# Kernel tuning notes

Hardware: AMD Instinct MI355X
Metric: run time of the kernel (lower is better)

Reference implementation:

```python
import jax, jax.numpy as jnp
import numpy as np

B, S, L, DM, DP, H, HT, NO = 1, 64, 256, 256, 128, 8, 4, 32
EPS = 1e-5


def _lin(key, din, dout):
    k1, k2 = jax.random.split(key)
    s = 1.0 / np.sqrt(din)
    w = jax.random.uniform(k1, (din, dout), minval=-s, maxval=s, dtype=jnp.float32)
    b = jax.random.uniform(k2, (dout,), minval=-s, maxval=s, dtype=jnp.float32)
    return w, b


def setup_inputs() -> dict:
    key = jax.random.key(0)
    ks = jax.random.split(key, 16)
    inp = {}
    inp['msa'] = jax.random.normal(ks[0], (B, S, L, DM), dtype=jnp.float32)
    inp['pair'] = jax.random.normal(ks[1], (B, L, L, DP), dtype=jnp.float32)
    # row attention
    inp['row_norm_g'] = jnp.ones((DM,), jnp.float32); inp['row_norm_b'] = jnp.zeros((DM,), jnp.float32)
    inp['row_qkv_w'], inp['row_qkv_b'] = _lin(ks[2], DM, 3 * DM)
    inp['row_out_w'], inp['row_out_b'] = _lin(ks[3], DM, DM)
    # column attention
    inp['col_norm_g'] = jnp.ones((DM,), jnp.float32); inp['col_norm_b'] = jnp.zeros((DM,), jnp.float32)
    inp['col_qkv_w'], inp['col_qkv_b'] = _lin(ks[4], DM, 3 * DM)
    inp['col_out_w'], inp['col_out_b'] = _lin(ks[5], DM, DM)
    inp['ff_norm_g'] = jnp.ones((DM,), jnp.float32); inp['ff_norm_b'] = jnp.zeros((DM,), jnp.float32)
    inp['ff_w1'], inp['ff_b1'] = _lin(ks[6], DM, 4 * DM)
    inp['ff_w2'], inp['ff_b2'] = _lin(ks[7], 4 * DM, DM)
    # outer product mean
    inp['op_norm_g'] = jnp.ones((DM,), jnp.float32); inp['op_norm_b'] = jnp.zeros((DM,), jnp.float32)
    inp['op_a_w'], inp['op_a_b'] = _lin(ks[8], DM, NO)
    inp['op_b_w'], inp['op_b_b'] = _lin(ks[9], DM, NO)
    inp['op_out_w'], inp['op_out_b'] = _lin(ks[10], NO * NO, DP)
    # triangle attention
    inp['tri_norm_g'] = jnp.ones((DP,), jnp.float32); inp['tri_norm_b'] = jnp.zeros((DP,), jnp.float32)
    inp['tri_qkv_w'], inp['tri_qkv_b'] = _lin(ks[11], DP, 3 * DP)
    inp['tri_out_w'], inp['tri_out_b'] = _lin(ks[12], DP, DP)
    return inp


def layer_norm(x, g, b):
    m = jnp.mean(x, axis=-1, keepdims=True)
    v = jnp.mean(jnp.square(x - m), axis=-1, keepdims=True)
    return (x - m) * jax.lax.rsqrt(v + EPS) * g + b


def mha(x, qkv_w, qkv_b, out_w, out_b, n_heads):
    # x: (..., n, d); attention over axis n. Dropout is eval-mode (identity).
    *lead, n, d = x.shape
    hd = d // n_heads
    qkv = x @ qkv_w + qkv_b
    q, k, v = jnp.split(qkv, 3, axis=-1)
    q = q.reshape(*lead, n, n_heads, hd)
    k = k.reshape(*lead, n, n_heads, hd)
    v = v.reshape(*lead, n, n_heads, hd)
    attn = jnp.einsum('...ihd,...jhd->...hij', q, k) * (hd ** -0.5)
    attn = jnp.clip(attn, -50.0, 50.0)
    attn = jax.nn.softmax(attn, axis=-1)
    out = jnp.einsum('...hij,...jhd->...ihd', attn, v).reshape(*lead, n, d)
    return out @ out_w + out_b


def reference(msa, pair,
              row_norm_g, row_norm_b, row_qkv_w, row_qkv_b, row_out_w, row_out_b,
              col_norm_g, col_norm_b, col_qkv_w, col_qkv_b, col_out_w, col_out_b,
              ff_norm_g, ff_norm_b, ff_w1, ff_b1, ff_w2, ff_b2,
              op_norm_g, op_norm_b, op_a_w, op_a_b, op_b_w, op_b_b, op_out_w, op_out_b,
              tri_norm_g, tri_norm_b, tri_qkv_w, tri_qkv_b, tri_out_w, tri_out_b):
    # row attention over seq_len axis
    msa = msa + mha(layer_norm(msa, row_norm_g, row_norm_b),
                    row_qkv_w, row_qkv_b, row_out_w, row_out_b, H)
    # column attention: transpose (b s n d) -> (b n s d), attend over n_seqs
    msa_t = jnp.swapaxes(msa, 1, 2)
    msa_t = msa_t + mha(layer_norm(msa_t, col_norm_g, col_norm_b),
                        col_qkv_w, col_qkv_b, col_out_w, col_out_b, H)
    msa = jnp.swapaxes(msa_t, 1, 2)
    # feed-forward
    h = layer_norm(msa, ff_norm_g, ff_norm_b)
    msa = msa + (jax.nn.relu(h @ ff_w1 + ff_b1) @ ff_w2 + ff_b2)
    # outer product mean: msa -> pair update
    m = layer_norm(msa, op_norm_g, op_norm_b)
    a = m @ op_a_w + op_a_b   # (b, s, L, NO)
    b_ = m @ op_b_w + op_b_b  # (b, s, L, NO)
    n_seqs = msa.shape[1]
    outer = jnp.einsum('bsic,bsjd->bijcd', a, b_) / float(n_seqs)  # (b, L, L, NO, NO)
    bsz, Ld = outer.shape[0], outer.shape[1]
    pair = pair + outer.reshape(bsz, Ld, Ld, NO * NO) @ op_out_w + op_out_b
    # triangle attention (row-wise attention over last L axis, 4 heads)
    pn = layer_norm(pair, tri_norm_g, tri_norm_b)
    pair = pair + mha(pn, tri_qkv_w, tri_qkv_b, tri_out_w, tri_out_b, HT)
    return msa, pair
```

## Files before the change

kernel.cpp:

```cpp
#include <hip/hip_runtime.h>
#include <hip/hip_bf16.h>


#define S_ 64
#define L_ 256
#define DM_ 256
#define DP_ 128
#define H_ 8
#define HT_ 4
#define NO_ 32

typedef __hip_bfloat16 bf16;
typedef short short4s __attribute__((ext_vector_type(4)));
typedef short short8 __attribute__((ext_vector_type(8)));
typedef float floatx4 __attribute__((ext_vector_type(4)));

__device__ __forceinline__ short f2bfs(float x) {
  union { float f; unsigned u; } v;
  v.f = x;
  unsigned r = (v.u + 0x7fffu + ((v.u >> 16) & 1u)) >> 16;
  return (short)r;
}

__global__ void k_ln(const float* __restrict__ src, bf16* __restrict__ dst,
                     const float* __restrict__ g, const float* __restrict__ bta, int D) {
  int row = blockIdx.x * 4 + (threadIdx.x >> 6);
  const float* x = src + (size_t)row * D;
  bf16* y = dst + (size_t)row * D;
  int t = threadIdx.x & 63;
  float v[4];
  int cnt = 0;
  float sum = 0.f;
  for (int e = t; e < D; e += 64) { float xv = x[e]; v[cnt++] = xv; sum += xv; }
  #pragma unroll
  for (int o = 32; o; o >>= 1) sum += __shfl_down(sum, o);
  sum = __shfl(sum, 0);
  float mean = sum / D;
  float var = 0.f;
  for (int k = 0; k < cnt; k++) { float d = v[k] - mean; var += d * d; }
  #pragma unroll
  for (int o = 32; o; o >>= 1) var += __shfl_down(var, o);
  var = __shfl(var, 0);
  float rstd = rsqrtf(var / D + 1e-5f);
  cnt = 0;
  for (int e = t; e < D; e += 64)
    y[e] = __float2bfloat16((v[cnt++] - mean) * rstd * g[e] + bta[e]);
}

struct WtJob { const float* W; bf16* Wt; int K; int N; int nblk; };
struct WtJobs { WtJob j[10]; };

__global__ void k_wt_all(WtJobs jobs) {
  __shared__ float tile[32][33];
  int b = blockIdx.x;
  int ji = 0;
  while (ji < 9 && b >= jobs.j[ji].nblk) { b -= jobs.j[ji].nblk; ji++; }
  const float* W = jobs.j[ji].W;
  bf16* Wt = jobs.j[ji].Wt;
  int K = jobs.j[ji].K, N = jobs.j[ji].N;
  int kt = K >> 5;
  int k0 = (b % kt) * 32, n0 = (b / kt) * 32;
  int tid = threadIdx.x;
  for (int e = tid; e < 1024; e += 256) {
    int r = e >> 5, c = e & 31;
    tile[r][c] = W[(size_t)(k0 + r) * N + (n0 + c)];
  }
  __syncthreads();
  for (int e = tid; e < 1024; e += 256) {
    int r = e >> 5, c = e & 31;
    Wt[(size_t)(n0 + r) * K + (k0 + c)] = __float2bfloat16(tile[c][r]);
  }
}

__global__ void k_wtopm(const float* __restrict__ W, bf16* __restrict__ Wt,
                        const float* __restrict__ ba, const float* __restrict__ bb,
                        float* __restrict__ bias_ab) {
  if (blockIdx.x == 0 && threadIdx.x < 64)
    bias_ab[threadIdx.x] = threadIdx.x < 32 ? ba[threadIdx.x] : bb[threadIdx.x - 32];
  int idx = blockIdx.x * 256 + threadIdx.x;
  int d = idx >> 10, kk = idx & 1023;
  int e = kk >> 5, c = kk & 31;
  Wt[idx] = __float2bfloat16(W[(size_t)(c * 32 + e) * 128 + d]);
}

__global__ void k_topm(const bf16* __restrict__ ab, bf16* __restrict__ a_t,
                       bf16* __restrict__ b_t) {
  __shared__ bf16 tile[64][34];
  int i = blockIdx.x;
  int y = blockIdx.y;
  bf16* out = y ? b_t : a_t;
  int tid = threadIdx.x;
  for (int e = tid; e < 64 * 32; e += 256) {
    int s = e >> 5, c = e & 31;
    tile[s][c] = ab[((size_t)s * L_ + i) * 64 + y * 32 + c];
  }
  __syncthreads();
  for (int e = tid; e < 64 * 32; e += 256) {
    int c = e >> 6, s = e & 63;
    out[((size_t)i * NO_ + c) * S_ + s] = tile[s][c];
  }
}

template<int MODE, int LNF>
__global__ void k_gemm64(const bf16* __restrict__ A, const bf16* __restrict__ Wt,
                         const float* __restrict__ bias, float* __restrict__ Cf,
                         bf16* __restrict__ Cb, const float* __restrict__ Csrc,
                         float* __restrict__ Cdup, int M, int N, int K, float scale,
                         const float* __restrict__ Af = nullptr,
                         const float* __restrict__ lng = nullptr,
                         const float* __restrict__ lnbt = nullptr) {
  __shared__ short As[64 * 64];
  __shared__ short Bs[64 * 64];
  __shared__ float sMean[64];
  __shared__ float sRstd[64];
  const int tid = threadIdx.x;
  const int nwg = gridDim.x * gridDim.y;
  const int wgid = blockIdx.y * gridDim.x + blockIdx.x;
  const int q = nwg >> 3, r8 = nwg & 7;
  const int xcd = wgid & 7, loc = wgid >> 3;
  const int swz = (xcd < r8 ? xcd * (q + 1) : r8 * (q + 1) + (xcd - r8) * q) + loc;
  const int by = swz / gridDim.x, bx = swz - by * gridDim.x;
  const int m0 = by * 64, n0 = bx * 64;
  const int w = tid >> 6, l = tid & 63;
  const int wm = (w >> 1) * 32, wn = (w & 1) * 32;
  const int lr = l & 15, lk = l >> 4;

  if (LNF) {
    int rr = tid >> 2, quad = tid & 3;
    const float* xr = Af + (size_t)(m0 + rr) * 256 + quad * 64;
    float s = 0.f, s2 = 0.f;
    #pragma unroll
    for (int ii = 0; ii < 16; ii++) {
      floatx4 x = *(const floatx4*)(xr + ii * 4);
      #pragma unroll
      for (int jj = 0; jj < 4; jj++) { s += x[jj]; s2 += x[jj] * x[jj]; }
    }
    #pragma unroll
    for (int o = 1; o <= 2; o <<= 1) { s += __shfl_xor(s, o); s2 += __shfl_xor(s2, o); }
    if (quad == 0) {
      float mean = s * 0.00390625f;
      float var = s2 * 0.00390625f - mean * mean;
      sMean[rr] = mean;
      sRstd[rr] = rsqrtf(var + 1e-5f);
    }
    __syncthreads();
  }

  floatx4 acc[2][2] = {};
  const short* Ash = (const short*)A;
  const short* Bsh = (const short*)Wt;
  for (int k0 = 0; k0 < K; k0 += 64) {
    if (LNF) {
      for (int e = tid; e < 512; e += 256) {
        int r = e >> 3, kg = e & 7;
        int kb = k0 + kg * 8;
        const float* src = Af + (size_t)(m0 + r) * 256 + kb;
        floatx4 x0 = *(const floatx4*)(src);
        floatx4 x1 = *(const floatx4*)(src + 4);
        float mean = sMean[r], rstd = sRstd[r];
        short8 v;
        #pragma unroll
        for (int jj = 0; jj < 4; jj++) {
          v[jj] = f2bfs((x0[jj] - mean) * rstd * lng[kb + jj] + lnbt[kb + jj]);
          v[jj + 4] = f2bfs((x1[jj] - mean) * rstd * lng[kb + 4 + jj] + lnbt[kb + 4 + jj]);
        }
        *(short8*)(&As[r * 64 + ((kg ^ (r & 7)) * 8)]) = v;
      }
    } else {
      for (int e = tid; e < 512; e += 256) {
        int r = e >> 3, kg = e & 7;
        short8 v = *(const short8*)(Ash + (size_t)(m0 + r) * K + k0 + kg * 8);
        *(short8*)(&As[r * 64 + ((kg ^ (r & 7)) * 8)]) = v;
      }
    }
    for (int e = tid; e < 512; e += 256) {
      int r = e >> 3, kg = e & 7;
      int n = n0 + r;
      short8 v = {0, 0, 0, 0, 0, 0, 0, 0};
      if (n < N) v = *(const short8*)(Bsh + (size_t)n * K + k0 + kg * 8);
      *(short8*)(&Bs[r * 64 + ((kg ^ (r & 7)) * 8)]) = v;
    }
    __syncthreads();
    #pragma unroll
    for (int kk = 0; kk < 2; kk++) {
      short8 af[2], bfr[2];
      #pragma unroll
      for (int mi = 0; mi < 2; mi++) {
        int row = wm + mi * 16 + lr;
        int kg = kk * 4 + lk;
        af[mi] = *(const short8*)(&As[row * 64 + ((kg ^ (row & 7)) * 8)]);
      }
      #pragma unroll
      for (int ni = 0; ni < 2; ni++) {
        int row = wn + ni * 16 + lr;
        int kg = kk * 4 + lk;
        bfr[ni] = *(const short8*)(&Bs[row * 64 + ((kg ^ (row & 7)) * 8)]);
      }
      #pragma unroll
      for (int mi = 0; mi < 2; mi++)
        #pragma unroll
        for (int ni = 0; ni < 2; ni++)
          acc[mi][ni] = __builtin_amdgcn_mfma_f32_16x16x32_bf16(af[mi], bfr[ni], acc[mi][ni], 0, 0, 0);
    }
    __syncthreads();
  }
  #pragma unroll
  for (int ni = 0; ni < 2; ni++) {
    int n = n0 + wn + ni * 16 + lr;
    if (n >= N) continue;
    float bv = bias ? bias[n] : 0.f;
    #pragma unroll
    for (int mi = 0; mi < 2; mi++) {
      int mbase = m0 + wm + mi * 16 + lk * 4;
      #pragma unroll
      for (int r = 0; r < 4; r++) {
        float v = acc[mi][ni][r] * scale + bv;
        size_t idx = (size_t)(mbase + r) * N + n;
        if (MODE == 0) Cf[idx] = v;
        else if (MODE == 1) Cf[idx] += v;
        else if (MODE == 2) Cb[idx] = __float2bfloat16(v);
        else if (MODE == 3) Cb[idx] = __float2bfloat16(fmaxf(v, 0.f));
        else if (MODE == 4) Cf[idx] = Csrc[idx] + v;
        else if (MODE == 5) { float t = Cf[idx] + v; Cf[idx] = t; Cdup[idx] = t; }
      }
    }
  }
}

__global__ __launch_bounds__(256) void k_opm_fused(
    const bf16* __restrict__ a_t, const bf16* __restrict__ b_t,
    const bf16* __restrict__ Wt, const float* __restrict__ bias,
    const float* __restrict__ pair_in, float* __restrict__ pair_out) {
  __shared__ short U[32 * 512];
  const int i = blockIdx.y;
  const int jg = blockIdx.x;
  const int tid = threadIdx.x;
  const int w = tid >> 6, l = tid & 63;
  const int lr = l & 15, lk = l >> 4;
  const short* at = (const short*)a_t;
  const short* bt = (const short*)b_t;
  const short* wt = (const short*)Wt;

  short8 af[2][2];
  #pragma unroll
  for (int kh = 0; kh < 2; kh++)
    #pragma unroll
    for (int ks = 0; ks < 2; ks++)
      af[kh][ks] = *(const short8*)(at + ((size_t)i * 32 + kh * 16 + lr) * 64 + ks * 32 + lk * 8);

  floatx4 pacc[2][2] = {};
  #pragma unroll
  for (int kh = 0; kh < 2; kh++) {
    #pragma unroll
    for (int sc = 0; sc < 2; sc++) {
      floatx4 uacc[8] = {};
      const size_t rowbase = ((size_t)(jg * 32 + sc * 16) << 5) + w * 128;
      #pragma unroll
      for (int ks = 0; ks < 2; ks++)
        #pragma unroll
        for (int nt = 0; nt < 8; nt++) {
          short8 bfr = *(const short8*)(bt + (rowbase + nt * 16 + lr) * 64 + ks * 32 + lk * 8);
          uacc[nt] = __builtin_amdgcn_mfma_f32_16x16x32_bf16(af[kh][ks], bfr, uacc[nt], 0, 0, 0);
        }
      #pragma unroll
      for (int nt = 0; nt < 8; nt++) {
        int npos = w * 128 + nt * 16 + lr;
        int jj = sc * 16 + (npos >> 5);
        int e = npos & 31;
        int g = e * 2 + (lk >> 1);
        int off = (lk & 1) * 4;
        short4s pk;
        pk.x = f2bfs(uacc[nt][0] * 0.015625f);
        pk.y = f2bfs(uacc[nt][1] * 0.015625f);
        pk.z = f2bfs(uacc[nt][2] * 0.015625f);
        pk.w = f2bfs(uacc[nt][3] * 0.015625f);
        *(short4s*)(&U[jj * 512 + ((g ^ (jj & 7)) << 3) + off]) = pk;
      }
    }
    __syncthreads();
    #pragma unroll 4
    for (int ks = 0; ks < 16; ks++) {
      short8 afp[2];
      #pragma unroll
      for (int mt = 0; mt < 2; mt++) {
        int row = mt * 16 + lr;
        int g = ks * 4 + lk;
        afp[mt] = *(const short8*)(&U[row * 512 + ((g ^ (row & 7)) << 3)]);
      }
      int wko = (ks * 2 + (lk >> 1)) * 32 + kh * 16 + (lk & 1) * 8;
      #pragma unroll
      for (int ntl = 0; ntl < 2; ntl++) {
        int d = (w * 2 + ntl) * 16 + lr;
        short8 bfr = *(const short8*)(wt + (size_t)d * 1024 + wko);
        #pragma unroll
        for (int mt = 0; mt < 2; mt++)
          pacc[mt][ntl] = __builtin_amdgcn_mfma_f32_16x16x32_bf16(afp[mt], bfr, pacc[mt][ntl], 0, 0, 0);
      }
    }
    __syncthreads();
  }
  int jbase = jg * 32;
  #pragma unroll
  for (int ntl = 0; ntl < 2; ntl++) {
    int d = (w * 2 + ntl) * 16 + lr;
    float bv = bias[d];
    #pragma unroll
    for (int mt = 0; mt < 2; mt++)
      #pragma unroll
      for (int r = 0; r < 4; r++) {
        int j = jbase + mt * 16 + lk * 4 + r;
        size_t idx = ((size_t)i * L_ + j) * DP_ + d;
        pair_out[idx] = pair_in[idx] + pacc[mt][ntl][r] + bv;
      }
  }
}

template<int N>
__global__ __launch_bounds__(256) void k_attn_mfma(
    const bf16* __restrict__ qkv, bf16* __restrict__ out, int dmodel,
    int tokStride, int leadStride, int otokStride, int oleadStride, float scale) {
  constexpr int NT = N / 16;
  constexpr int NK = N / 32;
  constexpr int NIC = N / 64;
  __shared__ short Ks[N * 32];
  __shared__ short Vt[N * 32];
  __shared__ short Qs[2048];
  __shared__ short P[64 * N];

  const int lead = blockIdx.x;
  const int h = blockIdx.y;
  const short* base = (const short*)qkv + (size_t)lead * leadStride;
  const int qoff = h * 32, koff = dmodel + h * 32, voff = 2 * dmodel + h * 32;
  const int tid = threadIdx.x;
  const int l = tid & 63, w = tid >> 6;
  const int lr = l & 15, lk = l >> 4;

  for (int e = tid; e < N * 4; e += 256) {
    int j = e >> 2, kg = e & 3;
    short8 v = *(const short8*)(base + (size_t)j * tokStride + koff + kg * 8);
    *(short8*)(&Ks[(kg * N + j) * 8]) = v;
  }
  for (int e = tid; e < N * 32; e += 256) {
    int j = e >> 5, d = e & 31;
    Vt[((j >> 5) * 4 + ((j >> 3) & 3)) * 256 + d * 8 + (j & 7)] = base[(size_t)j * tokStride + voff + d];
  }
  __syncthreads();

  for (int ic = 0; ic < NIC; ic++) {
    {
      int r = tid >> 2, kg = tid & 3;
      short8 v = *(const short8*)(base + (size_t)(ic * 64 + r) * tokStride + qoff + kg * 8);
      *(short8*)(&Qs[(kg * 64 + r) * 8]) = v;
    }
    short8 aq = *(const short8*)(&Qs[(lk * 64 + w * 16 + lr) * 8]);
    floatx4 sa[NT];
    #pragma unroll
    for (int t = 0; t < NT; t++) {
      short8 bk = *(const short8*)(&Ks[(lk * N + t * 16 + lr) * 8]);
      floatx4 z = {0.f, 0.f, 0.f, 0.f};
      sa[t] = __builtin_amdgcn_mfma_f32_16x16x32_bf16(aq, bk, z, 0, 0, 0);
    }

    float mrow[4] = {-1e30f, -1e30f, -1e30f, -1e30f};
    #pragma unroll
    for (int t = 0; t < NT; t++)
      #pragma unroll
      for (int r = 0; r < 4; r++) {
        float s = fminf(fmaxf(sa[t][r] * scale, -50.f), 50.f);
        sa[t][r] = s;
        mrow[r] = fmaxf(mrow[r], s);
      }
    #pragma unroll
    for (int o = 1; o <= 8; o <<= 1)
      #pragma unroll
      for (int r = 0; r < 4; r++) mrow[r] = fmaxf(mrow[r], __shfl_xor(mrow[r], o));
    float srow[4] = {0.f, 0.f, 0.f, 0.f};
    #pragma unroll
    for (int t = 0; t < NT; t++)
      #pragma unroll
      for (int r = 0; r < 4; r++) {
        float p = __expf(sa[t][r] - mrow[r]);
        sa[t][r] = p;
        srow[r] += p;
      }
    #pragma unroll
    for (int o = 1; o <= 8; o <<= 1)
      #pragma unroll
      for (int r = 0; r < 4; r++) srow[r] += __shfl_xor(srow[r], o);
    float inv[4];
    #pragma unroll
    for (int r = 0; r < 4; r++) inv[r] = 1.f / srow[r];

    #pragma unroll
    for (int t = 0; t < NT; t++) {
      int c = t * 16 + lr;
      int kstep = c >> 5, kslot = (c >> 3) & 3, u = c & 7;
      #pragma unroll
      for (int r = 0; r < 4; r++) {
        int row = w * 16 + lk * 4 + r;
        P[((kstep * 4 + kslot) * 64 + row) * 8 + u] = f2bfs(sa[t][r] * inv[r]);
      }
    }

    floatx4 oacc[2] = {{0.f,0.f,0.f,0.f},{0.f,0.f,0.f,0.f}};
    #pragma unroll
    for (int ks = 0; ks < NK; ks++) {
      short8 ap = *(const short8*)(&P[((ks * 4 + lk) * 64 + w * 16 + lr) * 8]);
      #pragma unroll
      for (int ct = 0; ct < 2; ct++) {
        short8 bv = *(const short8*)(&Vt[((ks * 4 + lk) * 32 + ct * 16 + lr) * 8]);
        oacc[ct] = __builtin_amdgcn_mfma_f32_16x16x32_bf16(ap, bv, oacc[ct], 0, 0, 0);
      }
    }
    bf16* ob = out + (size_t)lead * oleadStride + h * 32;
    #pragma unroll
    for (int ct = 0; ct < 2; ct++)
      #pragma unroll
      for (int r = 0; r < 4; r++) {
        int tok = ic * 64 + w * 16 + lk * 4 + r;
        ob[(size_t)tok * otokStride + ct * 16 + lr] = __float2bfloat16(oacc[ct][r]);
      }
  }
}

extern "C" void kernel_launch(void* const* d_in, const int* in_sizes, int n_in,
                              void* d_out, int out_size, void* d_ws, size_t ws_size,
                              hipStream_t stream) {
  const float* msa_in    = (const float*)d_in[0];
  const float* pair_in   = (const float*)d_in[1];
  const float* row_ng    = (const float*)d_in[2];
  const float* row_nb    = (const float*)d_in[3];
  const float* row_qkv_w = (const float*)d_in[4];
  const float* row_qkv_b = (const float*)d_in[5];
  const float* row_out_w = (const float*)d_in[6];
  const float* row_out_b = (const float*)d_in[7];
  const float* col_ng    = (const float*)d_in[8];
  const float* col_nb    = (const float*)d_in[9];
  const float* col_qkv_w = (const float*)d_in[10];
  const float* col_qkv_b = (const float*)d_in[11];
  const float* col_out_w = (const float*)d_in[12];
  const float* col_out_b = (const float*)d_in[13];
  const float* ff_ng     = (const float*)d_in[14];
  const float* ff_nb     = (const float*)d_in[15];
  const float* ff_w1     = (const float*)d_in[16];
  const float* ff_b1     = (const float*)d_in[17];
  const float* ff_w2     = (const float*)d_in[18];
  const float* ff_b2     = (const float*)d_in[19];
  const float* op_ng     = (const float*)d_in[20];
  const float* op_nb     = (const float*)d_in[21];
  const float* op_a_w    = (const float*)d_in[22];
  const float* op_a_b    = (const float*)d_in[23];
  const float* op_b_w    = (const float*)d_in[24];
  const float* op_b_b    = (const float*)d_in[25];
  const float* op_out_w  = (const float*)d_in[26];
  const float* op_out_b  = (const float*)d_in[27];
  const float* tri_ng    = (const float*)d_in[28];
  const float* tri_nb    = (const float*)d_in[29];
  const float* tri_qkv_w = (const float*)d_in[30];
  const float* tri_qkv_b = (const float*)d_in[31];
  const float* tri_out_w = (const float*)d_in[32];
  const float* tri_out_b = (const float*)d_in[33];

  const int MT = S_ * L_;
  const int PT = L_ * L_;

  char* ws = (char*)d_ws;
  float* msa_f  = (float*)(ws);
  float* pair_f = (float*)(ws + 16777216);
  char*  X      = ws + 50331648;
  bf16*  ln_b   = (bf16*)(ws + 100663296);
  bf16*  ao_b   = (bf16*)(ws + 117440512);
  bf16*  ab_buf = (bf16*)(ws + 134217728);
  bf16*  a_t    = (bf16*)(ws + 136314880);
  bf16*  b_t    = (bf16*)(ws + 137363456);
  bf16*  wts    = (bf16*)(ws + 138412032);
  float* bias_ab = (float*)(ws + 141557760);

  bf16* row_qkv_wt = wts;
  bf16* col_qkv_wt = row_qkv_wt + 196608;
  bf16* row_out_wt = col_qkv_wt + 196608;
  bf16* col_out_wt = row_out_wt + 65536;
  bf16* ff_w1t     = col_out_wt + 65536;
  bf16* ff_w2t     = ff_w1t + 262144;
  bf16* op_ab_wt   = ff_w2t + 262144;
  bf16* op_out_wt  = op_ab_wt + 16384;
  bf16* tri_qkv_wt = op_out_wt + 131072;
  bf16* tri_out_wt = tri_qkv_wt + 49152;

  bf16* qkv_bf = (bf16*)X;
  bf16* ffh    = (bf16*)X;

  float* dout_msa  = (float*)d_out;
  float* dout_pair = (float*)d_out + (size_t)MT * DM_;

  const float scale = 0.17677669529663687f;

  WtJobs jobs;
  jobs.j[0] = {row_qkv_w, row_qkv_wt, 256, 768, 192};
  jobs.j[1] = {col_qkv_w, col_qkv_wt, 256, 768, 192};
  jobs.j[2] = {row_out_w, row_out_wt, 256, 256, 64};
  jobs.j[3] = {col_out_w, col_out_wt, 256, 256, 64};
  jobs.j[4] = {ff_w1, ff_w1t, 256, 1024, 256};
  jobs.j[5] = {ff_w2, ff_w2t, 1024, 256, 256};
  jobs.j[6] = {op_a_w, op_ab_wt, 256, 32, 8};
  jobs.j[7] = {op_b_w, op_ab_wt + 32 * 256, 256, 32, 8};
  jobs.j[8] = {tri_qkv_w, tri_qkv_wt, 128, 384, 48};
  jobs.j[9] = {tri_out_w, tri_out_wt, 128, 128, 16};
  k_wt_all<<<1104, 256, 0, stream>>>(jobs);
  k_wtopm<<<512, 256, 0, stream>>>(op_out_w, op_out_wt, op_a_b, op_b_b, bias_ab);

  k_ln<<<MT / 4, 256, 0, stream>>>(msa_in, ln_b, row_ng, row_nb, DM_);
  k_gemm64<2,0><<<dim3(12, 256), 256, 0, stream>>>(ln_b, row_qkv_wt, row_qkv_b, nullptr, qkv_bf, nullptr, nullptr, MT, 768, 256, 1.f);
  k_attn_mfma<256><<<dim3(S_, H_), 256, 0, stream>>>(qkv_bf, ao_b, DM_, 768, L_ * 768, DM_, L_ * DM_, scale);
  k_gemm64<4,0><<<dim3(4, 256), 256, 0, stream>>>(ao_b, row_out_wt, row_out_b, msa_f, nullptr, msa_in, nullptr, MT, DM_, DM_, 1.f);

  k_ln<<<MT / 4, 256, 0, stream>>>(msa_f, ln_b, col_ng, col_nb, DM_);
  k_gemm64<2,0><<<dim3(12, 256), 256, 0, stream>>>(ln_b, col_qkv_wt, col_qkv_b, nullptr, qkv_bf, nullptr, nullptr, MT, 768, 256, 1.f);
  k_attn_mfma<64><<<dim3(L_, H_), 256, 0, stream>>>(qkv_bf, ao_b, DM_, L_ * 768, 768, L_ * DM_, DM_, scale);
  k_gemm64<1,0><<<dim3(4, 256), 256, 0, stream>>>(ao_b, col_out_wt, col_out_b, msa_f, nullptr, nullptr, nullptr, MT, DM_, DM_, 1.f);

  k_ln<<<MT / 4, 256, 0, stream>>>(msa_f, ln_b, ff_ng, ff_nb, DM_);
  k_gemm64<3,0><<<dim3(16, 256), 256, 0, stream>>>(ln_b, ff_w1t, ff_b1, nullptr, ffh, nullptr, nullptr, MT, 1024, 256, 1.f);
  k_gemm64<5,0><<<dim3(4, 256), 256, 0, stream>>>(ffh, ff_w2t, ff_b2, msa_f, nullptr, nullptr, dout_msa, MT, DM_, 1024, 1.f);

  k_gemm64<2,1><<<dim3(1, 256), 256, 0, stream>>>(nullptr, op_ab_wt, bias_ab, nullptr, ab_buf, nullptr, nullptr, MT, 64, 256, 1.f, msa_f, op_ng, op_nb);
  k_topm<<<dim3(L_, 2), 256, 0, stream>>>(ab_buf, a_t, b_t);
  k_opm_fused<<<dim3(8, L_), 256, 0, stream>>>(a_t, b_t, op_out_wt, op_out_b, pair_in, pair_f);

  k_ln<<<PT / 4, 256, 0, stream>>>(pair_f, ln_b, tri_ng, tri_nb, DP_);
  k_gemm64<2,0><<<dim3(6, 1024), 256, 0, stream>>>(ln_b, tri_qkv_wt, tri_qkv_b, nullptr, qkv_bf, nullptr, nullptr, PT, 384, DP_, 1.f);
  k_attn_mfma<256><<<dim3(L_, HT_), 256, 0, stream>>>(qkv_bf, ao_b, DP_, 384, L_ * 384, DP_, L_ * DP_, scale);
  k_gemm64<4,0><<<dim3(2, 1024), 256, 0, stream>>>(ao_b, tri_out_wt, tri_out_b, dout_pair, nullptr, pair_f, nullptr, PT, DP_, DP_, 1.f);
}
```

Before: 438.9 us.

## Fuse OPM transpose into projection GEMM epilogue and widen OPM kernel to 512 threads

The outer-product-mean a/b projection GEMM now writes its bf16 output directly in the transposed (i, c, s) layout, so the separate k_topm transpose kernel and its intermediate buffer are gone. The fused OPM kernel now runs with 8 waves per block instead of 4, and each wave handles half as many tiles. This is meant to save one launch and one round trip through global memory, and to raise occupancy and parallelism in the OPM kernel. The cost is scattered, uncoalesced 2-byte stores in the GEMM epilogue and heavier LDS and synchronisation contention among more waves.

```diff
diff --git a/kernel.cpp b/kernel.cpp
--- a/kernel.cpp
+++ b/kernel.cpp
@@ -83,24 +83,6 @@
   Wt[idx] = __float2bfloat16(W[(size_t)(c * 32 + e) * 128 + d]);
 }
 
-__global__ void k_topm(const bf16* __restrict__ ab, bf16* __restrict__ a_t,
-                       bf16* __restrict__ b_t) {
-  __shared__ bf16 tile[64][34];
-  int i = blockIdx.x;
-  int y = blockIdx.y;
-  bf16* out = y ? b_t : a_t;
-  int tid = threadIdx.x;
-  for (int e = tid; e < 64 * 32; e += 256) {
-    int s = e >> 5, c = e & 31;
-    tile[s][c] = ab[((size_t)s * L_ + i) * 64 + y * 32 + c];
-  }
-  __syncthreads();
-  for (int e = tid; e < 64 * 32; e += 256) {
-    int c = e >> 6, s = e & 63;
-    out[((size_t)i * NO_ + c) * S_ + s] = tile[s][c];
-  }
-}
-
 template<int MODE, int LNF>
 __global__ void k_gemm64(const bf16* __restrict__ A, const bf16* __restrict__ Wt,
                          const float* __restrict__ bias, float* __restrict__ Cf,
@@ -222,12 +204,19 @@
         else if (MODE == 3) Cb[idx] = __float2bfloat16(fmaxf(v, 0.f));
         else if (MODE == 4) Cf[idx] = Csrc[idx] + v;
         else if (MODE == 5) { float t = Cf[idx] + v; Cf[idx] = t; Cdup[idx] = t; }
-      }
-    }
-  }
-}
-
-__global__ __launch_bounds__(256) void k_opm_fused(
+        else if (MODE == 6) {
+          int m = mbase + r;
+          int s = m >> 8, i2 = m & 255;
+          int y = n >> 5, c = n & 31;
+          bf16* outp = y ? (bf16*)Cdup : Cb;
+          outp[((size_t)i2 * NO_ + c) * S_ + s] = __float2bfloat16(v);
+        }
+      }
+    }
+  }
+}
+
+__global__ __launch_bounds__(512) void k_opm_fused(
     const bf16* __restrict__ a_t, const bf16* __restrict__ b_t,
     const bf16* __restrict__ Wt, const float* __restrict__ bias,
     const float* __restrict__ pair_in, float* __restrict__ pair_out) {
@@ -248,23 +237,23 @@
     for (int ks = 0; ks < 2; ks++)
       af[kh][ks] = *(const short8*)(at + ((size_t)i * 32 + kh * 16 + lr) * 64 + ks * 32 + lk * 8);
 
-  floatx4 pacc[2][2] = {};
+  floatx4 pacc[2] = {};
   #pragma unroll
   for (int kh = 0; kh < 2; kh++) {
     #pragma unroll
     for (int sc = 0; sc < 2; sc++) {
-      floatx4 uacc[8] = {};
-      const size_t rowbase = ((size_t)(jg * 32 + sc * 16) << 5) + w * 128;
+      floatx4 uacc[4] = {};
+      const size_t rowbase = ((size_t)(jg * 32 + sc * 16) << 5) + w * 64;
       #pragma unroll
       for (int ks = 0; ks < 2; ks++)
         #pragma unroll
-        for (int nt = 0; nt < 8; nt++) {
+        for (int nt = 0; nt < 4; nt++) {
           short8 bfr = *(const short8*)(bt + (rowbase + nt * 16 + lr) * 64 + ks * 32 + lk * 8);
           uacc[nt] = __builtin_amdgcn_mfma_f32_16x16x32_bf16(af[kh][ks], bfr, uacc[nt], 0, 0, 0);
         }
       #pragma unroll
-      for (int nt = 0; nt < 8; nt++) {
-        int npos = w * 128 + nt * 16 + lr;
+      for (int nt = 0; nt < 4; nt++) {
+        int npos = w * 64 + nt * 16 + lr;
         int jj = sc * 16 + (npos >> 5);
         int e = npos & 31;
         int g = e * 2 + (lk >> 1);
@@ -288,31 +277,25 @@
         afp[mt] = *(const short8*)(&U[row * 512 + ((g ^ (row & 7)) << 3)]);
       }
       int wko = (ks * 2 + (lk >> 1)) * 32 + kh * 16 + (lk & 1) * 8;
-      #pragma unroll
-      for (int ntl = 0; ntl < 2; ntl++) {
-        int d = (w * 2 + ntl) * 16 + lr;
-        short8 bfr = *(const short8*)(wt + (size_t)d * 1024 + wko);
-        #pragma unroll
-        for (int mt = 0; mt < 2; mt++)
-          pacc[mt][ntl] = __builtin_amdgcn_mfma_f32_16x16x32_bf16(afp[mt], bfr, pacc[mt][ntl], 0, 0, 0);
-      }
+      int d = w * 16 + lr;
+      short8 bfr = *(const short8*)(wt + (size_t)d * 1024 + wko);
+      #pragma unroll
+      for (int mt = 0; mt < 2; mt++)
+        pacc[mt] = __builtin_amdgcn_mfma_f32_16x16x32_bf16(afp[mt], bfr, pacc[mt], 0, 0, 0);
     }
     __syncthreads();
   }
   int jbase = jg * 32;
+  int d = w * 16 + lr;
+  float bv = bias[d];
   #pragma unroll
-  for (int ntl = 0; ntl < 2; ntl++) {
-    int d = (w * 2 + ntl) * 16 + lr;
-    float bv = bias[d];
-    #pragma unroll
-    for (int mt = 0; mt < 2; mt++)
-      #pragma unroll
-      for (int r = 0; r < 4; r++) {
-        int j = jbase + mt * 16 + lk * 4 + r;
-        size_t idx = ((size_t)i * L_ + j) * DP_ + d;
-        pair_out[idx] = pair_in[idx] + pacc[mt][ntl][r] + bv;
-      }
-  }
+  for (int mt = 0; mt < 2; mt++)
+    #pragma unroll
+    for (int r = 0; r < 4; r++) {
+      int j = jbase + mt * 16 + lk * 4 + r;
+      size_t idx = ((size_t)i * L_ + j) * DP_ + d;
+      pair_out[idx] = pair_in[idx] + pacc[mt][r] + bv;
+    }
 }
 
 template<int N>
@@ -470,7 +453,6 @@
   char*  X      = ws + 50331648;
   bf16*  ln_b   = (bf16*)(ws + 100663296);
   bf16*  ao_b   = (bf16*)(ws + 117440512);
-  bf16*  ab_buf = (bf16*)(ws + 134217728);
   bf16*  a_t    = (bf16*)(ws + 136314880);
   bf16*  b_t    = (bf16*)(ws + 137363456);
   bf16*  wts    = (bf16*)(ws + 138412032);
@@ -523,9 +505,8 @@
   k_gemm64<3,0><<<dim3(16, 256), 256, 0, stream>>>(ln_b, ff_w1t, ff_b1, nullptr, ffh, nullptr, nullptr, MT, 1024, 256, 1.f);
   k_gemm64<5,0><<<dim3(4, 256), 256, 0, stream>>>(ffh, ff_w2t, ff_b2, msa_f, nullptr, nullptr, dout_msa, MT, DM_, 1024, 1.f);
 
-  k_gemm64<2,1><<<dim3(1, 256), 256, 0, stream>>>(nullptr, op_ab_wt, bias_ab, nullptr, ab_buf, nullptr, nullptr, MT, 64, 256, 1.f, msa_f, op_ng, op_nb);
-  k_topm<<<dim3(L_, 2), 256, 0, stream>>>(ab_buf, a_t, b_t);
-  k_opm_fused<<<dim3(8, L_), 256, 0, stream>>>(a_t, b_t, op_out_wt, op_out_b, pair_in, pair_f);
+  k_gemm64<6,1><<<dim3(1, 256), 256, 0, stream>>>(nullptr, op_ab_wt, bias_ab, nullptr, a_t, nullptr, (float*)b_t, MT, 64, 256, 1.f, msa_f, op_ng, op_nb);
+  k_opm_fused<<<dim3(8, L_), 512, 0, stream>>>(a_t, b_t, op_out_wt, op_out_b, pair_in, pair_f);
 
   k_ln<<<PT / 4, 256, 0, stream>>>(pair_f, ln_b, tri_ng, tri_nb, DP_);
   k_gemm64<2,0><<<dim3(6, 1024), 256, 0, stream>>>(ln_b, tri_qkv_wt, tri_qkv_b, nullptr, qkv_bf, nullptr, nullptr, PT, 384, DP_, 1.f);
```

Measured after the change: 428.1 us. 2.5% less time.
